# Optimization experiments

Hardware: AMD Instinct MI355X
Metric: run time of the kernel (lower is better)

The kernel has to match this reference:

```python
import jax, jax.numpy as jnp
import numpy as np

NUM_HEADS = 4
KERNEL = 7
DILATION = 1
EMBED = 128
CTX = 256
RANK = 8
HEAD_DIM = EMBED // NUM_HEADS
SCALE = HEAD_DIM ** (-0.5)


def setup_inputs() -> dict:
    key = jax.random.key(0)
    ks = jax.random.split(key, 16)
    B, H, W = 4, 64, 64
    inp = {
        "x": jax.random.normal(ks[0], (B, H, W, EMBED), jnp.float32),
        "context": jax.random.normal(ks[1], (B, CTX), jnp.float32),
        # base QKV linear (torch Linear: y = x @ W.T + b)
        "Wqkv": jax.random.normal(ks[2], (3 * EMBED, EMBED), jnp.float32) * 0.02,
        "bqkv": jax.random.normal(ks[3], (3 * EMBED,), jnp.float32) * 0.02,
        # bilinear LoRA params (init scale 0.01 as in source)
        "A": jax.random.normal(ks[4], (EMBED, RANK), jnp.float32) * 0.01,
        "Blora": jax.random.normal(ks[5], (CTX, RANK), jnp.float32) * 0.01,
        "Vlora": jax.random.normal(ks[6], (3 * EMBED, RANK), jnp.float32) * 0.01,
        # gate MLP: Linear(ctx,16) -> ReLU -> Linear(16,1) -> Sigmoid
        "g1w": jax.random.normal(ks[7], (16, CTX), jnp.float32) * 0.05,
        "g1b": jnp.zeros((16,), jnp.float32),
        "g2w": jnp.full((1, 16), -5.0, jnp.float32) * 0.0 + jax.random.normal(ks[8], (1, 16), jnp.float32) * 0.01 - 5.0 / 16.0,
        "g2b": jnp.full((1,), -5.0, jnp.float32),
        # output projection
        "Wproj": jax.random.normal(ks[9], (EMBED, EMBED), jnp.float32) * 0.02,
        "bproj": jnp.zeros((EMBED,), jnp.float32),
    }
    return inp


def _windows(t, H, W):
    # t: [B, nh, H+2p, W+2p, d] -> [B, nh, H, W, K^2, d]
    ws = []
    for i in range(KERNEL):
        for j in range(KERNEL):
            ws.append(t[:, :, i * DILATION:i * DILATION + H, j * DILATION:j * DILATION + W, :])
    return jnp.stack(ws, axis=4)


def reference(x, context, Wqkv, bqkv, A, Blora, Vlora, g1w, g1b, g2w, g2b, Wproj, bproj):
    B, H, W, C = x.shape
    nh, hd = NUM_HEADS, HEAD_DIM
    # context-modulated QKV: base + alpha * ((xA) * (cB)) V^T
    base = x @ Wqkv.T + bqkv                                   # [B,H,W,3C]
    c_proj = context @ Blora                                   # [B,r]
    delta = ((x @ A) * c_proj[:, None, None, :]) @ Vlora.T     # [B,H,W,3C]
    alpha = jax.nn.sigmoid(jax.nn.relu(context @ g1w.T + g1b) @ g2w.T + g2b)  # [B,1]
    qkv = base + alpha[:, None, None, :] * delta               # [B,H,W,3C]

    qkv = qkv.reshape(B, H, W, 3, nh, hd)
    qkv = jnp.transpose(qkv, (3, 0, 4, 1, 2, 5))               # [3,B,nh,H,W,hd]
    q, k, v = qkv[0], qkv[1], qkv[2]

    pad = DILATION * (KERNEL - 1) // 2
    pw = ((0, 0), (0, 0), (pad, pad), (pad, pad), (0, 0))
    k_p = jnp.pad(k, pw)
    v_p = jnp.pad(v, pw)
    kw = _windows(k_p, H, W)                                   # [B,nh,H,W,K2,hd]
    vw = _windows(v_p, H, W)

    attn = jnp.einsum('bnijd,bnijkd->bnijk', q, kw) * SCALE    # [B,nh,H,W,K2]
    attn = jax.nn.softmax(attn, axis=-1)
    out = jnp.einsum('bnijk,bnijkd->bnijd', attn, vw)          # [B,nh,H,W,hd]

    out = jnp.transpose(out, (0, 2, 3, 1, 4)).reshape(B, H, W, C)
    out = out @ Wproj.T + bproj
    return out
```

## Files before the change

kernel.cpp:

```cpp
#include <hip/hip_runtime.h>
#include <cstddef>

#define CTXDIM 256
#define RANK 8
#define SCALE 0.17677669529663687f
#define WSTRIDE 136

#define XH0 0
#define WF0 26656
#define QS0 35360
#define KL0 44064
#define VT0 61984
#define SMSZ 78368
#define KHEAD 8960
#define VHEAD2 8192

typedef _Float16 half8 __attribute__((ext_vector_type(8)));
typedef _Float16 half2_t __attribute__((ext_vector_type(2)));
typedef float floatx4 __attribute__((ext_vector_type(4)));
typedef float floatx16 __attribute__((ext_vector_type(16)));
typedef int intx4 __attribute__((ext_vector_type(4)));

struct Params {
  const float *x, *ctx, *Wqkv, *bqkv, *A, *Blora, *Vlora;
  const float *g1w, *g1b, *g2w, *g2b, *Wproj, *bproj;
  float* out;
};

__device__ __forceinline__ void compute_cal(const Params& p, int tid,
                                            float* cal_s) {
  const int b = tid >> 6, lane = tid & 63;
  const float c0 = p.ctx[b * CTXDIM + lane];
  const float c1 = p.ctx[b * CTXDIM + 64 + lane];
  const float c2 = p.ctx[b * CTXDIM + 128 + lane];
  const float c3 = p.ctx[b * CTXDIM + 192 + lane];
  float cp[RANK];
#pragma unroll
  for (int r = 0; r < RANK; ++r) {
    float q = c0 * p.Blora[lane * RANK + r] + c1 * p.Blora[(64 + lane) * RANK + r] +
              c2 * p.Blora[(128 + lane) * RANK + r] + c3 * p.Blora[(192 + lane) * RANK + r];
#pragma unroll
    for (int s = 32; s; s >>= 1) q += __shfl_xor(q, s, 64);
    cp[r] = q;
  }
  float gacc = 0.f;
#pragma unroll
  for (int h = 0; h < 16; ++h) {
    float q = c0 * p.g1w[h * CTXDIM + lane] + c1 * p.g1w[h * CTXDIM + 64 + lane] +
              c2 * p.g1w[h * CTXDIM + 128 + lane] + c3 * p.g1w[h * CTXDIM + 192 + lane];
#pragma unroll
    for (int s = 32; s; s >>= 1) q += __shfl_xor(q, s, 64);
    gacc += fmaxf(q + p.g1b[h], 0.f) * p.g2w[h];
  }
  if (lane == 0) {
    const float alpha = 1.f / (1.f + __expf(-(gacc + p.g2b[0])));
#pragma unroll
    for (int r = 0; r < RANK; ++r) cal_s[b * RANK + r] = alpha * cp[r];
  }
}

__device__ __forceinline__ void stage_rows_f16(const float* __restrict__ src,
                                               _Float16* dst, int tid) {
  const int row = tid >> 2;
  const int c0 = (tid & 3) * 32;
  const float* sp = src + (size_t)row * 128 + c0;
  _Float16* dp = dst + row * WSTRIDE + c0;
#pragma unroll
  for (int i = 0; i < 4; ++i) {
    const float4 a = *(const float4*)(sp + i * 8);
    const float4 b = *(const float4*)(sp + i * 8 + 4);
    half8 o;
    o[0] = (_Float16)a.x; o[1] = (_Float16)a.y;
    o[2] = (_Float16)a.z; o[3] = (_Float16)a.w;
    o[4] = (_Float16)b.x; o[5] = (_Float16)b.y;
    o[6] = (_Float16)b.z; o[7] = (_Float16)b.w;
    *(half8*)(dp + i * 8) = o;
  }
}

__device__ __forceinline__ int vta(int d, int k) {
  const int sig = (d + (d >> 3)) & 7;
  return d * 256 + (((k >> 3) ^ sig) << 3) + (k & 7);
}

__device__ __forceinline__ int packh(float x, float y) {
  half2_t h;
  h[0] = (_Float16)x;
  h[1] = (_Float16)y;
  return __builtin_bit_cast(int, h);
}

template <int MT0>
__device__ __forceinline__ floatx16 attn_wave(const _Float16* kls,
                                              const _Float16* vtl,
                                              half8 qb0, half8 qb1,
                                              int m31, int l5, int pi, int pj) {
  const floatx16 zz = {0.f,0.f,0.f,0.f,0.f,0.f,0.f,0.f,
                       0.f,0.f,0.f,0.f,0.f,0.f,0.f,0.f};
  floatx16 acc[5];
#pragma unroll
  for (int mt = 0; mt < 5; ++mt) {
    const int Mt = MT0 + mt;
    const half8 ka0 = *(const half8*)&kls[(Mt * 32 + m31) * 40 + l5 * 8];
    const half8 ka1 = *(const half8*)&kls[(Mt * 32 + m31) * 40 + 16 + l5 * 8];
    floatx16 a = zz;
    a = __builtin_amdgcn_mfma_f32_32x32x16_f16(ka0, qb0, a, 0, 0, 0);
    a = __builtin_amdgcn_mfma_f32_32x32x16_f16(ka1, qb1, a, 0, 0, 0);
    acc[mt] = a;
  }

  bool vR[14];
#pragma unroll
  for (int i = 0; i < 14; ++i) vR[i] = (unsigned)(i - pi) < 7u;
  bool vC[8];
#pragma unroll
  for (int c8 = 0; c8 < 8; ++c8) {
    const int hcv = (c8 & 3) + 8 * (c8 >> 2) + 4 * l5;
    vC[c8] = (unsigned)(hcv - pj) < 7u;
  }

  float mxp[4] = {-1e30f, -1e30f, -1e30f, -1e30f};
#pragma unroll
  for (int mt = 0; mt < 5; ++mt) {
#pragma unroll
    for (int reg = 0; reg < 16; ++reg) {
      const bool v = vR[2 * (MT0 + mt) + (reg >> 3)] &&
                     vC[(reg & 3) + 4 * ((reg >> 2) & 1)];
      const float x = v ? acc[mt][reg] : -1e30f;
      acc[mt][reg] = x;
      mxp[reg & 3] = fmaxf(mxp[reg & 3], x);
    }
  }
  float mx = fmaxf(fmaxf(mxp[0], mxp[1]), fmaxf(mxp[2], mxp[3]));
  mx = fmaxf(mx, __shfl_xor(mx, 32, 64));

  const float SC2 = SCALE * 1.4426950408889634f;
  float sp[4] = {0.f, 0.f, 0.f, 0.f};
#pragma unroll
  for (int mt = 0; mt < 5; ++mt) {
#pragma unroll
    for (int reg = 0; reg < 16; ++reg) {
      const float pv = exp2f((acc[mt][reg] - mx) * SC2);
      acc[mt][reg] = pv;
      sp[reg & 3] += pv;
    }
  }
  float sum = (sp[0] + sp[1]) + (sp[2] + sp[3]);
  sum += __shfl_xor(sum, 32, 64);
  const float inv = 1.f / sum;

  floatx16 oacc = zz;
  const int sigd = (m31 + (m31 >> 3)) & 7;
  const int vbase = m31 * 256;
#pragma unroll
  for (int kk = 0; kk < 10; ++kk) {
    const int ks = MT0 * 2 + kk;
    const int mt = (ks >> 1) - MT0;
    const int r8 = 8 * (ks & 1);
    const int E00 = packh(acc[mt][r8 + 0] * inv, acc[mt][r8 + 1] * inv);
    const int E01 = packh(acc[mt][r8 + 2] * inv, acc[mt][r8 + 3] * inv);
    const int E10 = packh(acc[mt][r8 + 4] * inv, acc[mt][r8 + 5] * inv);
    const int E11 = packh(acc[mt][r8 + 6] * inv, acc[mt][r8 + 7] * inv);
    const int R00 = __shfl_xor(E00, 32, 64);
    const int R01 = __shfl_xor(E01, 32, 64);
    const int R10 = __shfl_xor(E10, 32, 64);
    const int R11 = __shfl_xor(E11, 32, 64);
    const int A0 = l5 ? R10 : E00;
    const int A1 = l5 ? R11 : E01;
    const int A2 = l5 ? E10 : R00;
    const int A3 = l5 ? E11 : R01;
    const intx4 ai = {A0, A1, A2, A3};
    const half8 af = __builtin_bit_cast(half8, ai);
    const half8 vb = *(const half8*)&vtl[vbase + (((2 * ks + l5) ^ sigd) << 3)];
    oacc = __builtin_amdgcn_mfma_f32_32x32x16_f16(af, vb, oacc, 0, 0, 0);
  }
  return oacc;
}

__global__ __launch_bounds__(256, 1) void mono_kernel(Params p) {
  __shared__ __align__(16) _Float16 sm[SMSZ];
  __shared__ float cal_s[32];

  const int bid = blockIdx.x;
  const int tj = bid & 7;
  const int ti = (bid >> 3) & 7;
  const int b  = bid >> 6;
  const int tid = threadIdx.x;
  const int lane = tid & 63;
  const int w = tid >> 6;
  const int m31 = lane & 31;
  const int l5 = lane >> 5;
  const int i0 = ti * 8 - 3;
  const int j0 = tj * 8 - 3;

  _Float16* xh    = sm + XH0;
  _Float16* wfold = sm + WF0;
  _Float16* qs    = sm + QS0;
  _Float16* kls   = sm + KL0;
  _Float16* vtl   = sm + VT0;

  compute_cal(p, tid, cal_s);

  for (int idx = tid; idx < 896; idx += 256) {
    const int d = idx & 31;
    const int kk = idx >> 5;
    const int k = (kk >> 1) * 16 + 14 + (kk & 1);
    const int a = vta(d, k);
    vtl[a] = (_Float16)0.f;
    vtl[VHEAD2 + a] = (_Float16)0.f;
  }

  for (int s = tid; s < 3136; s += 256) {
    const int pp = s >> 4;
    const int d8 = (s & 15) * 8;
    const int hr = pp / 14;
    const int hc = pp - hr * 14;
    const int ii = i0 + hr;
    const int jj = j0 + hc;
    half8 o = {0, 0, 0, 0, 0, 0, 0, 0};
    if ((unsigned)ii < 64u && (unsigned)jj < 64u) {
      const float* sp = p.x + (size_t)(b * 4096 + ii * 64 + jj) * 128 + d8;
      const float4 a = *(const float4*)sp;
      const float4 c = *(const float4*)(sp + 4);
      o[0] = (_Float16)a.x; o[1] = (_Float16)a.y;
      o[2] = (_Float16)a.z; o[3] = (_Float16)a.w;
      o[4] = (_Float16)c.x; o[5] = (_Float16)c.y;
      o[6] = (_Float16)c.z; o[7] = (_Float16)c.w;
    }
    *(half8*)&xh[pp * 136 + d8] = o;
  }

  const int kq = tid & 127;
  const int hgrp = tid >> 7;
  const float4 a0 = *(const float4*)&p.A[kq * RANK];
  const float4 a1 = *(const float4*)&p.A[kq * RANK + 4];
  const float* cb = &cal_s[b * RANK];

  __syncthreads();

  const float t0 = a0.x * cb[0], t1 = a0.y * cb[1];
  const float t2 = a0.z * cb[2], t3 = a0.w * cb[3];
  const float t4 = a1.x * cb[4], t5 = a1.y * cb[5];
  const float t6 = a1.z * cb[6], t7 = a1.w * cb[7];

  const floatx16 zz = {0.f,0.f,0.f,0.f,0.f,0.f,0.f,0.f,
                       0.f,0.f,0.f,0.f,0.f,0.f,0.f,0.f};
  const int sigd = (m31 + (m31 >> 3)) & 7;

  auto FOLD = [&](int n0) {
#pragma unroll
    for (int rr = 0; rr < 32; ++rr) {
      const int row = hgrp * 32 + rr;
      const int o = n0 + row;
      const float4 v0 = *(const float4*)&p.Vlora[o * RANK];
      const float4 v1 = *(const float4*)&p.Vlora[o * RANK + 4];
      float d = t0 * v0.x;
      d = fmaf(t1, v0.y, d);
      d = fmaf(t2, v0.z, d);
      d = fmaf(t3, v0.w, d);
      d = fmaf(t4, v1.x, d);
      d = fmaf(t5, v1.y, d);
      d = fmaf(t6, v1.z, d);
      d = fmaf(t7, v1.w, d);
      wfold[row * WSTRIDE + kq] = (_Float16)(p.Wqkv[o * 128 + kq] + d);
    }
  };

  auto QGEMM = [&](int i) {
    const int n0 = i * 64;
    const int mt = w + 1;
    const float bq0 = p.bqkv[n0 + m31];
    const float bq1 = p.bqkv[n0 + 32 + m31];
    floatx16 c0 = zz, c1 = zz;
    const _Float16* ar  = &xh[(mt * 32 + m31) * 136 + l5 * 8];
    const _Float16* b0r = &wfold[m31 * WSTRIDE + l5 * 8];
    const _Float16* b1r = &wfold[(32 + m31) * WSTRIDE + l5 * 8];
#pragma unroll
    for (int ks = 0; ks < 8; ++ks) {
      const half8 a  = *(const half8*)(ar + ks * 16);
      const half8 f0 = *(const half8*)(b0r + ks * 16);
      const half8 f1 = *(const half8*)(b1r + ks * 16);
      c0 = __builtin_amdgcn_mfma_f32_32x32x16_f16(a, f0, c0, 0, 0, 0);
      c1 = __builtin_amdgcn_mfma_f32_32x32x16_f16(a, f1, c1, 0, 0, 0);
    }
#pragma unroll
    for (int reg = 0; reg < 16; ++reg) {
      const int rowlin = mt * 32 + (reg & 3) + 8 * (reg >> 2) + 4 * l5;
      const int hr = rowlin / 14;
      const int hc = rowlin - hr * 14;
      if ((unsigned)(hr - 3) < 8u && (unsigned)(hc - 3) < 8u) {
        const int px = (hr - 3) * 8 + (hc - 3);
        qs[px * 136 + n0 + m31] = (_Float16)(c0[reg] + bq0);
        qs[px * 136 + n0 + 32 + m31] = (_Float16)(c1[reg] + bq1);
      }
    }
  };

  auto KVGEMM = [&](int i) {
    const int n0 = i * 64;
    const bool isK = (i < 4);
    const float bh0 = p.bqkv[n0 + m31];
    const float bh1 = p.bqkv[n0 + 32 + m31];
#pragma unroll
    for (int mtslot = 0; mtslot < 2; ++mtslot) {
      const int mt = w + 4 * mtslot;
      if (mt < 7) {
        floatx16 c0 = zz, c1 = zz;
        const _Float16* ar  = &xh[(mt * 32 + m31) * 136 + l5 * 8];
        const _Float16* b0r = &wfold[m31 * WSTRIDE + l5 * 8];
        const _Float16* b1r = &wfold[(32 + m31) * WSTRIDE + l5 * 8];
#pragma unroll
        for (int ks = 0; ks < 8; ++ks) {
          const half8 a  = *(const half8*)(ar + ks * 16);
          const half8 f0 = *(const half8*)(b0r + ks * 16);
          const half8 f1 = *(const half8*)(b1r + ks * 16);
          c0 = __builtin_amdgcn_mfma_f32_32x32x16_f16(a, f0, c0, 0, 0, 0);
          c1 = __builtin_amdgcn_mfma_f32_32x32x16_f16(a, f1, c1, 0, 0, 0);
        }
#pragma unroll
        for (int reg = 0; reg < 16; ++reg) {
          const int rowlin = mt * 32 + (reg & 3) + 8 * (reg >> 2) + 4 * l5;
          if (rowlin < 196) {
            const int hr = rowlin / 14;
            const int hc = rowlin - hr * 14;
            const int hp = hr * 16 + hc;
            const bool okimg = (unsigned)(i0 + hr) < 64u &&
                               (unsigned)(j0 + hc) < 64u;
            const float v0 = okimg ? c0[reg] + bh0 : 0.f;
            const float v1 = okimg ? c1[reg] + bh1 : 0.f;
            if (isK) {
              kls[hp * 40 + m31] = (_Float16)v0;
              kls[KHEAD + hp * 40 + m31] = (_Float16)v1;
            } else {
              const int off = (((hp >> 3) ^ sigd) << 3) | (hp & 7);
              vtl[m31 * 256 + off] = (_Float16)v0;
              vtl[VHEAD2 + m31 * 256 + off] = (_Float16)v1;
            }
          }
        }
      }
    }
  };

  FOLD(0);   __syncthreads(); QGEMM(0);  __syncthreads();
  FOLD(64);  __syncthreads(); QGEMM(1);  __syncthreads();
  FOLD(128); __syncthreads(); KVGEMM(2); __syncthreads();
  FOLD(256); __syncthreads(); KVGEMM(4); __syncthreads();

  const int hlq = w >> 1;
  const int half = w & 1;
  const int pixA = half * 32 + m31;
  const int piA = pixA >> 3, pjA = pixA & 7;
  const _Float16* kpp = kls + hlq * KHEAD;
  const _Float16* vpp = vtl + hlq * VHEAD2;

  floatx16 oP1;
  {
    const int hh = hlq;
    const half8 qb0 = *(const half8*)&qs[pixA * 136 + hh * 32 + l5 * 8];
    const half8 qb1 = *(const half8*)&qs[pixA * 136 + hh * 32 + 16 + l5 * 8];
    oP1 = half ? attn_wave<2>(kpp, vpp, qb0, qb1, m31, l5, piA, pjA)
               : attn_wave<0>(kpp, vpp, qb0, qb1, m31, l5, piA, pjA);
  }
  __syncthreads();

  FOLD(192); __syncthreads(); KVGEMM(3); __syncthreads();
  FOLD(320); __syncthreads(); KVGEMM(5); __syncthreads();

  floatx16 oP2;
  {
    const int hh = 2 + hlq;
    const half8 qb0 = *(const half8*)&qs[pixA * 136 + hh * 32 + l5 * 8];
    const half8 qb1 = *(const half8*)&qs[pixA * 136 + hh * 32 + 16 + l5 * 8];
    oP2 = half ? attn_wave<2>(kpp, vpp, qb0, qb1, m31, l5, piA, pjA)
               : attn_wave<0>(kpp, vpp, qb0, qb1, m31, l5, piA, pjA);
  }
  __syncthreads();

  _Float16* at_s = sm + KL0;
  _Float16* wsh  = sm + KL0 + 64 * WSTRIDE;
#pragma unroll
  for (int reg = 0; reg < 16; ++reg) {
    const int rowM = (reg & 3) + 8 * (reg >> 2) + 4 * l5;
    const int pr = half * 32 + rowM;
    at_s[pr * WSTRIDE + hlq * 32 + m31] = (_Float16)oP1[reg];
    at_s[pr * WSTRIDE + (2 + hlq) * 32 + m31] = (_Float16)oP2[reg];
  }
  stage_rows_f16(p.Wproj, wsh, tid);
  stage_rows_f16(p.Wproj + 64 * 128, wsh + 64 * WSTRIDE, tid);
  __syncthreads();

  const int r = lane & 15;
  const int quad = lane >> 4;
  const _Float16* ap = at_s + (w * 16 + r) * WSTRIDE + quad * 8;
  const _Float16* bp = wsh + r * WSTRIDE + quad * 8;
  floatx4 acc[8];
#pragma unroll
  for (int nt = 0; nt < 8; ++nt) acc[nt] = (floatx4){0.f, 0.f, 0.f, 0.f};
#pragma unroll
  for (int kc = 0; kc < 4; ++kc) {
    const half8 a = *(const half8*)(ap + kc * 32);
#pragma unroll
    for (int nt = 0; nt < 8; ++nt) {
      const half8 bf = *(const half8*)(bp + nt * 16 * WSTRIDE + kc * 32);
      acc[nt] = __builtin_amdgcn_mfma_f32_16x16x32_f16(a, bf, acc[nt], 0, 0, 0);
    }
  }

  const int rbase = b * 4096 + (ti * 8 + w * 2 + (quad >> 1)) * 64 +
                    tj * 8 + (quad & 1) * 4;
  float bv[8];
#pragma unroll
  for (int nt = 0; nt < 8; ++nt) bv[nt] = p.bproj[nt * 16 + r];
#pragma unroll
  for (int reg = 0; reg < 4; ++reg) {
    float* cp = p.out + (size_t)(rbase + reg) * 128;
#pragma unroll
    for (int nt = 0; nt < 8; ++nt)
      cp[nt * 16 + r] = acc[nt][reg] + bv[nt];
  }
}

extern "C" void kernel_launch(void* const* d_in, const int* in_sizes, int n_in,
                              void* d_out, int out_size, void* d_ws, size_t ws_size,
                              hipStream_t stream) {
  Params hp;
  hp.x     = (const float*)d_in[0];
  hp.ctx   = (const float*)d_in[1];
  hp.Wqkv  = (const float*)d_in[2];
  hp.bqkv  = (const float*)d_in[3];
  hp.A     = (const float*)d_in[4];
  hp.Blora = (const float*)d_in[5];
  hp.Vlora = (const float*)d_in[6];
  hp.g1w   = (const float*)d_in[7];
  hp.g1b   = (const float*)d_in[8];
  hp.g2w   = (const float*)d_in[9];
  hp.g2b   = (const float*)d_in[10];
  hp.Wproj = (const float*)d_in[11];
  hp.bproj = (const float*)d_in[12];
  hp.out   = (float*)d_out;

  mono_kernel<<<256, 256, 0, stream>>>(hp);
}
```

Before: 51.87 us.

## Double block to 512 threads, keep x rows in registers, run all heads' attention at once

The block grows from 256 to 512 threads (8 waves). The halo x tile is loaded straight into per-wave registers as fp16 MFMA A-fragments rather than staged in shared memory, which frees LDS. That space is used to keep K and V for all four heads at once, with the fourth V head parked in the reused fold buffer, so attention runs once across 8 waves instead of in two 4-wave passes. The fold, Q GEMM and projection work are split across the extra waves. This raises register pressure, since two 8-entry half8 x-row arrays plus saved V values must be held, and adds several cross-phase buffer-reuse dependencies.

New measurement: 46.80 us. 1.11x faster.

```diff
diff --git a/kernel.cpp b/kernel.cpp
--- a/kernel.cpp
+++ b/kernel.cpp
@@ -6,14 +6,13 @@
 #define SCALE 0.17677669529663687f
 #define WSTRIDE 136
 
-#define XH0 0
-#define WF0 26656
-#define QS0 35360
-#define KL0 44064
-#define VT0 61984
-#define SMSZ 78368
+#define WF0 0
+#define QS0 8704
+#define KL0 17408
+#define VT0 53248
+#define SMSZ 77824
 #define KHEAD 8960
-#define VHEAD2 8192
+#define VHEAD 8192
 
 typedef _Float16 half8 __attribute__((ext_vector_type(8)));
 typedef _Float16 half2_t __attribute__((ext_vector_type(2)));
@@ -27,40 +26,8 @@
   float* out;
 };
 
-__device__ __forceinline__ void compute_cal(const Params& p, int tid,
-                                            float* cal_s) {
-  const int b = tid >> 6, lane = tid & 63;
-  const float c0 = p.ctx[b * CTXDIM + lane];
-  const float c1 = p.ctx[b * CTXDIM + 64 + lane];
-  const float c2 = p.ctx[b * CTXDIM + 128 + lane];
-  const float c3 = p.ctx[b * CTXDIM + 192 + lane];
-  float cp[RANK];
-#pragma unroll
-  for (int r = 0; r < RANK; ++r) {
-    float q = c0 * p.Blora[lane * RANK + r] + c1 * p.Blora[(64 + lane) * RANK + r] +
-              c2 * p.Blora[(128 + lane) * RANK + r] + c3 * p.Blora[(192 + lane) * RANK + r];
-#pragma unroll
-    for (int s = 32; s; s >>= 1) q += __shfl_xor(q, s, 64);
-    cp[r] = q;
-  }
-  float gacc = 0.f;
-#pragma unroll
-  for (int h = 0; h < 16; ++h) {
-    float q = c0 * p.g1w[h * CTXDIM + lane] + c1 * p.g1w[h * CTXDIM + 64 + lane] +
-              c2 * p.g1w[h * CTXDIM + 128 + lane] + c3 * p.g1w[h * CTXDIM + 192 + lane];
-#pragma unroll
-    for (int s = 32; s; s >>= 1) q += __shfl_xor(q, s, 64);
-    gacc += fmaxf(q + p.g1b[h], 0.f) * p.g2w[h];
-  }
-  if (lane == 0) {
-    const float alpha = 1.f / (1.f + __expf(-(gacc + p.g2b[0])));
-#pragma unroll
-    for (int r = 0; r < RANK; ++r) cal_s[b * RANK + r] = alpha * cp[r];
-  }
-}
-
-__device__ __forceinline__ void stage_rows_f16(const float* __restrict__ src,
-                                               _Float16* dst, int tid) {
+__device__ __forceinline__ void stage_rows_f16_512(const float* __restrict__ src,
+                                                   _Float16* dst, int tid) {
   const int row = tid >> 2;
   const int c0 = (tid & 3) * 32;
   const float* sp = src + (size_t)row * 128 + c0;
@@ -177,9 +144,9 @@
   return oacc;
 }
 
-__global__ __launch_bounds__(256, 1) void mono_kernel(Params p) {
+__global__ __launch_bounds__(512, 1) void mono_kernel(Params p) {
   __shared__ __align__(16) _Float16 sm[SMSZ];
-  __shared__ float cal_s[32];
+  __shared__ float cal_s[8];
 
   const int bid = blockIdx.x;
   const int tj = bid & 7;
@@ -193,64 +160,101 @@
   const int i0 = ti * 8 - 3;
   const int j0 = tj * 8 - 3;
 
-  _Float16* xh    = sm + XH0;
   _Float16* wfold = sm + WF0;
   _Float16* qs    = sm + QS0;
   _Float16* kls   = sm + KL0;
   _Float16* vtl   = sm + VT0;
 
-  compute_cal(p, tid, cal_s);
-
-  for (int idx = tid; idx < 896; idx += 256) {
-    const int d = idx & 31;
-    const int kk = idx >> 5;
+  const floatx16 zz = {0.f,0.f,0.f,0.f,0.f,0.f,0.f,0.f,
+                       0.f,0.f,0.f,0.f,0.f,0.f,0.f,0.f};
+  const int sigd = (m31 + (m31 >> 3)) & 7;
+
+  auto load_xrow = [&](int rowlin, half8* xr) {
+#pragma unroll
+    for (int ks = 0; ks < 8; ++ks) xr[ks] = (half8){0, 0, 0, 0, 0, 0, 0, 0};
+    if (rowlin < 196) {
+      const int hr = rowlin / 14;
+      const int hc = rowlin - hr * 14;
+      const int ii = i0 + hr;
+      const int jj = j0 + hc;
+      if ((unsigned)ii < 64u && (unsigned)jj < 64u) {
+        const float* xp = p.x + (size_t)(b * 4096 + ii * 64 + jj) * 128 + l5 * 8;
+#pragma unroll
+        for (int ks = 0; ks < 8; ++ks) {
+          const float4 a = *(const float4*)(xp + ks * 16);
+          const float4 c = *(const float4*)(xp + ks * 16 + 4);
+          half8 o;
+          o[0] = (_Float16)a.x; o[1] = (_Float16)a.y;
+          o[2] = (_Float16)a.z; o[3] = (_Float16)a.w;
+          o[4] = (_Float16)c.x; o[5] = (_Float16)c.y;
+          o[6] = (_Float16)c.z; o[7] = (_Float16)c.w;
+          xr[ks] = o;
+        }
+      }
+    }
+  };
+
+  const int mtq = (w & 3) + 1;
+  const int chq = w >> 2;
+  half8 xrq[8];
+  load_xrow(mtq * 32 + m31, xrq);
+
+  if (w == 0) {
+    const float c0 = p.ctx[b * CTXDIM + lane];
+    const float c1 = p.ctx[b * CTXDIM + 64 + lane];
+    const float c2 = p.ctx[b * CTXDIM + 128 + lane];
+    const float c3 = p.ctx[b * CTXDIM + 192 + lane];
+    float cp[RANK];
+#pragma unroll
+    for (int r = 0; r < RANK; ++r) {
+      float q = c0 * p.Blora[lane * RANK + r] + c1 * p.Blora[(64 + lane) * RANK + r] +
+                c2 * p.Blora[(128 + lane) * RANK + r] + c3 * p.Blora[(192 + lane) * RANK + r];
+#pragma unroll
+      for (int s = 32; s; s >>= 1) q += __shfl_xor(q, s, 64);
+      cp[r] = q;
+    }
+    float gacc = 0.f;
+#pragma unroll
+    for (int h = 0; h < 16; ++h) {
+      float q = c0 * p.g1w[h * CTXDIM + lane] + c1 * p.g1w[h * CTXDIM + 64 + lane] +
+                c2 * p.g1w[h * CTXDIM + 128 + lane] + c3 * p.g1w[h * CTXDIM + 192 + lane];
+#pragma unroll
+      for (int s = 32; s; s >>= 1) q += __shfl_xor(q, s, 64);
+      gacc += fmaxf(q + p.g1b[h], 0.f) * p.g2w[h];
+    }
+    if (lane == 0) {
+      const float alpha = 1.f / (1.f + __expf(-(gacc + p.g2b[0])));
+#pragma unroll
+      for (int r = 0; r < RANK; ++r) cal_s[r] = alpha * cp[r];
+    }
+  }
+
+  for (int idx = tid; idx < 2688; idx += 512) {
+    const int hd = idx / 896;
+    const int r2 = idx - hd * 896;
+    const int d = r2 & 31;
+    const int kk = r2 >> 5;
     const int k = (kk >> 1) * 16 + 14 + (kk & 1);
-    const int a = vta(d, k);
-    vtl[a] = (_Float16)0.f;
-    vtl[VHEAD2 + a] = (_Float16)0.f;
-  }
-
-  for (int s = tid; s < 3136; s += 256) {
-    const int pp = s >> 4;
-    const int d8 = (s & 15) * 8;
-    const int hr = pp / 14;
-    const int hc = pp - hr * 14;
-    const int ii = i0 + hr;
-    const int jj = j0 + hc;
-    half8 o = {0, 0, 0, 0, 0, 0, 0, 0};
-    if ((unsigned)ii < 64u && (unsigned)jj < 64u) {
-      const float* sp = p.x + (size_t)(b * 4096 + ii * 64 + jj) * 128 + d8;
-      const float4 a = *(const float4*)sp;
-      const float4 c = *(const float4*)(sp + 4);
-      o[0] = (_Float16)a.x; o[1] = (_Float16)a.y;
-      o[2] = (_Float16)a.z; o[3] = (_Float16)a.w;
-      o[4] = (_Float16)c.x; o[5] = (_Float16)c.y;
-      o[6] = (_Float16)c.z; o[7] = (_Float16)c.w;
-    }
-    *(half8*)&xh[pp * 136 + d8] = o;
+    vtl[hd * VHEAD + vta(d, k)] = (_Float16)0.f;
   }
 
   const int kq = tid & 127;
   const int hgrp = tid >> 7;
   const float4 a0 = *(const float4*)&p.A[kq * RANK];
   const float4 a1 = *(const float4*)&p.A[kq * RANK + 4];
-  const float* cb = &cal_s[b * RANK];
 
   __syncthreads();
 
+  const float* cb = cal_s;
   const float t0 = a0.x * cb[0], t1 = a0.y * cb[1];
   const float t2 = a0.z * cb[2], t3 = a0.w * cb[3];
   const float t4 = a1.x * cb[4], t5 = a1.y * cb[5];
   const float t6 = a1.z * cb[6], t7 = a1.w * cb[7];
 
-  const floatx16 zz = {0.f,0.f,0.f,0.f,0.f,0.f,0.f,0.f,
-                       0.f,0.f,0.f,0.f,0.f,0.f,0.f,0.f};
-  const int sigd = (m31 + (m31 >> 3)) & 7;
-
   auto FOLD = [&](int n0) {
 #pragma unroll
-    for (int rr = 0; rr < 32; ++rr) {
-      const int row = hgrp * 32 + rr;
+    for (int rr = 0; rr < 16; ++rr) {
+      const int row = hgrp * 16 + rr;
       const int o = n0 + row;
       const float4 v0 = *(const float4*)&p.Vlora[o * RANK];
       const float4 v1 = *(const float4*)&p.Vlora[o * RANK + 4];
@@ -268,155 +272,156 @@
 
   auto QGEMM = [&](int i) {
     const int n0 = i * 64;
-    const int mt = w + 1;
-    const float bq0 = p.bqkv[n0 + m31];
-    const float bq1 = p.bqkv[n0 + 32 + m31];
-    floatx16 c0 = zz, c1 = zz;
-    const _Float16* ar  = &xh[(mt * 32 + m31) * 136 + l5 * 8];
-    const _Float16* b0r = &wfold[m31 * WSTRIDE + l5 * 8];
-    const _Float16* b1r = &wfold[(32 + m31) * WSTRIDE + l5 * 8];
+    const int nc = n0 + chq * 32 + m31;
+    const float bq = p.bqkv[nc];
+    floatx16 c = zz;
+    const _Float16* br = &wfold[(chq * 32 + m31) * WSTRIDE + l5 * 8];
 #pragma unroll
     for (int ks = 0; ks < 8; ++ks) {
-      const half8 a  = *(const half8*)(ar + ks * 16);
-      const half8 f0 = *(const half8*)(b0r + ks * 16);
-      const half8 f1 = *(const half8*)(b1r + ks * 16);
-      c0 = __builtin_amdgcn_mfma_f32_32x32x16_f16(a, f0, c0, 0, 0, 0);
-      c1 = __builtin_amdgcn_mfma_f32_32x32x16_f16(a, f1, c1, 0, 0, 0);
+      const half8 f = *(const half8*)(br + ks * 16);
+      c = __builtin_amdgcn_mfma_f32_32x32x16_f16(xrq[ks], f, c, 0, 0, 0);
     }
 #pragma unroll
     for (int reg = 0; reg < 16; ++reg) {
-      const int rowlin = mt * 32 + (reg & 3) + 8 * (reg >> 2) + 4 * l5;
+      const int rowlin = mtq * 32 + (reg & 3) + 8 * (reg >> 2) + 4 * l5;
       const int hr = rowlin / 14;
       const int hc = rowlin - hr * 14;
       if ((unsigned)(hr - 3) < 8u && (unsigned)(hc - 3) < 8u) {
         const int px = (hr - 3) * 8 + (hc - 3);
-        qs[px * 136 + n0 + m31] = (_Float16)(c0[reg] + bq0);
-        qs[px * 136 + n0 + 32 + m31] = (_Float16)(c1[reg] + bq1);
+        qs[px * 136 + nc] = (_Float16)(c[reg] + bq);
       }
     }
   };
 
-  auto KVGEMM = [&](int i) {
-    const int n0 = i * 64;
-    const bool isK = (i < 4);
+  FOLD(0);   __syncthreads(); QGEMM(0); __syncthreads();
+  FOLD(64);  __syncthreads(); QGEMM(1); __syncthreads();
+
+  half8 xrkv[8];
+  load_xrow(w * 32 + m31, xrkv);
+  floatx16 v3save = zz;
+
+  auto KVGEMM = [&](int it) {
+    const int n0 = it * 64;
     const float bh0 = p.bqkv[n0 + m31];
     const float bh1 = p.bqkv[n0 + 32 + m31];
-#pragma unroll
-    for (int mtslot = 0; mtslot < 2; ++mtslot) {
-      const int mt = w + 4 * mtslot;
-      if (mt < 7) {
-        floatx16 c0 = zz, c1 = zz;
-        const _Float16* ar  = &xh[(mt * 32 + m31) * 136 + l5 * 8];
-        const _Float16* b0r = &wfold[m31 * WSTRIDE + l5 * 8];
-        const _Float16* b1r = &wfold[(32 + m31) * WSTRIDE + l5 * 8];
-#pragma unroll
-        for (int ks = 0; ks < 8; ++ks) {
-          const half8 a  = *(const half8*)(ar + ks * 16);
-          const half8 f0 = *(const half8*)(b0r + ks * 16);
-          const half8 f1 = *(const half8*)(b1r + ks * 16);
-          c0 = __builtin_amdgcn_mfma_f32_32x32x16_f16(a, f0, c0, 0, 0, 0);
-          c1 = __builtin_amdgcn_mfma_f32_32x32x16_f16(a, f1, c1, 0, 0, 0);
-        }
-#pragma unroll
-        for (int reg = 0; reg < 16; ++reg) {
-          const int rowlin = mt * 32 + (reg & 3) + 8 * (reg >> 2) + 4 * l5;
-          if (rowlin < 196) {
-            const int hr = rowlin / 14;
-            const int hc = rowlin - hr * 14;
-            const int hp = hr * 16 + hc;
-            const bool okimg = (unsigned)(i0 + hr) < 64u &&
-                               (unsigned)(j0 + hc) < 64u;
-            const float v0 = okimg ? c0[reg] + bh0 : 0.f;
-            const float v1 = okimg ? c1[reg] + bh1 : 0.f;
-            if (isK) {
-              kls[hp * 40 + m31] = (_Float16)v0;
-              kls[KHEAD + hp * 40 + m31] = (_Float16)v1;
-            } else {
-              const int off = (((hp >> 3) ^ sigd) << 3) | (hp & 7);
-              vtl[m31 * 256 + off] = (_Float16)v0;
-              vtl[VHEAD2 + m31 * 256 + off] = (_Float16)v1;
-            }
+    if (w < 7) {
+      floatx16 c0 = zz, c1 = zz;
+      const _Float16* b0r = &wfold[m31 * WSTRIDE + l5 * 8];
+      const _Float16* b1r = &wfold[(32 + m31) * WSTRIDE + l5 * 8];
+#pragma unroll
+      for (int ks = 0; ks < 8; ++ks) {
+        const half8 f0 = *(const half8*)(b0r + ks * 16);
+        const half8 f1 = *(const half8*)(b1r + ks * 16);
+        c0 = __builtin_amdgcn_mfma_f32_32x32x16_f16(xrkv[ks], f0, c0, 0, 0, 0);
+        c1 = __builtin_amdgcn_mfma_f32_32x32x16_f16(xrkv[ks], f1, c1, 0, 0, 0);
+      }
+#pragma unroll
+      for (int reg = 0; reg < 16; ++reg) {
+        const int rowlin = w * 32 + (reg & 3) + 8 * (reg >> 2) + 4 * l5;
+        if (rowlin < 196) {
+          const int hr = rowlin / 14;
+          const int hc = rowlin - hr * 14;
+          const int hp = hr * 16 + hc;
+          const bool ok = (unsigned)(i0 + hr) < 64u && (unsigned)(j0 + hc) < 64u;
+          const float v0 = ok ? c0[reg] + bh0 : 0.f;
+          const float v1 = ok ? c1[reg] + bh1 : 0.f;
+          const int off = (((hp >> 3) ^ sigd) << 3) | (hp & 7);
+          if (it == 2) {
+            kls[hp * 40 + m31] = (_Float16)v0;
+            kls[KHEAD + hp * 40 + m31] = (_Float16)v1;
+          } else if (it == 3) {
+            kls[2 * KHEAD + hp * 40 + m31] = (_Float16)v0;
+            kls[3 * KHEAD + hp * 40 + m31] = (_Float16)v1;
+          } else if (it == 4) {
+            vtl[m31 * 256 + off] = (_Float16)v0;
+            vtl[VHEAD + m31 * 256 + off] = (_Float16)v1;
+          } else {
+            vtl[2 * VHEAD + m31 * 256 + off] = (_Float16)v0;
+            v3save[reg] = v1;
           }
         }
       }
     }
   };
 
-  FOLD(0);   __syncthreads(); QGEMM(0);  __syncthreads();
-  FOLD(64);  __syncthreads(); QGEMM(1);  __syncthreads();
   FOLD(128); __syncthreads(); KVGEMM(2); __syncthreads();
+  FOLD(192); __syncthreads(); KVGEMM(3); __syncthreads();
   FOLD(256); __syncthreads(); KVGEMM(4); __syncthreads();
-
-  const int hlq = w >> 1;
-  const int half = w & 1;
-  const int pixA = half * 32 + m31;
+  FOLD(320); __syncthreads(); KVGEMM(5); __syncthreads();
+
+  for (int idx = tid; idx < 896; idx += 512) {
+    const int d = idx & 31;
+    const int kk = idx >> 5;
+    const int k = (kk >> 1) * 16 + 14 + (kk & 1);
+    wfold[vta(d, k)] = (_Float16)0.f;
+  }
+  if (w < 7) {
+#pragma unroll
+    for (int reg = 0; reg < 16; ++reg) {
+      const int rowlin = w * 32 + (reg & 3) + 8 * (reg >> 2) + 4 * l5;
+      if (rowlin < 196) {
+        const int hr = rowlin / 14;
+        const int hc = rowlin - hr * 14;
+        const int hp = hr * 16 + hc;
+        const int off = (((hp >> 3) ^ sigd) << 3) | (hp & 7);
+        wfold[m31 * 256 + off] = (_Float16)v3save[reg];
+      }
+    }
+  }
+  __syncthreads();
+
+  const int hh = w >> 1;
+  const int half_ = w & 1;
+  const int pixA = half_ * 32 + m31;
   const int piA = pixA >> 3, pjA = pixA & 7;
-  const _Float16* kpp = kls + hlq * KHEAD;
-  const _Float16* vpp = vtl + hlq * VHEAD2;
-
-  floatx16 oP1;
-  {
-    const int hh = hlq;
-    const half8 qb0 = *(const half8*)&qs[pixA * 136 + hh * 32 + l5 * 8];
-    const half8 qb1 = *(const half8*)&qs[pixA * 136 + hh * 32 + 16 + l5 * 8];
-    oP1 = half ? attn_wave<2>(kpp, vpp, qb0, qb1, m31, l5, piA, pjA)
-               : attn_wave<0>(kpp, vpp, qb0, qb1, m31, l5, piA, pjA);
-  }
+  const half8 qb0 = *(const half8*)&qs[pixA * 136 + hh * 32 + l5 * 8];
+  const half8 qb1 = *(const half8*)&qs[pixA * 136 + hh * 32 + 16 + l5 * 8];
+  const _Float16* kpp = kls + hh * KHEAD;
+  const _Float16* vpp = (hh < 3) ? (vtl + hh * VHEAD) : wfold;
+
+  const floatx16 oA = half_ ? attn_wave<2>(kpp, vpp, qb0, qb1, m31, l5, piA, pjA)
+                            : attn_wave<0>(kpp, vpp, qb0, qb1, m31, l5, piA, pjA);
   __syncthreads();
 
-  FOLD(192); __syncthreads(); KVGEMM(3); __syncthreads();
-  FOLD(320); __syncthreads(); KVGEMM(5); __syncthreads();
-
-  floatx16 oP2;
-  {
-    const int hh = 2 + hlq;
-    const half8 qb0 = *(const half8*)&qs[pixA * 136 + hh * 32 + l5 * 8];
-    const half8 qb1 = *(const half8*)&qs[pixA * 136 + hh * 32 + 16 + l5 * 8];
-    oP2 = half ? attn_wave<2>(kpp, vpp, qb0, qb1, m31, l5, piA, pjA)
-               : attn_wave<0>(kpp, vpp, qb0, qb1, m31, l5, piA, pjA);
-  }
-  __syncthreads();
-
-  _Float16* at_s = sm + KL0;
-  _Float16* wsh  = sm + KL0 + 64 * WSTRIDE;
+  _Float16* at_s = kls;
+  _Float16* wsh  = kls + 64 * WSTRIDE;
 #pragma unroll
   for (int reg = 0; reg < 16; ++reg) {
     const int rowM = (reg & 3) + 8 * (reg >> 2) + 4 * l5;
-    const int pr = half * 32 + rowM;
-    at_s[pr * WSTRIDE + hlq * 32 + m31] = (_Float16)oP1[reg];
-    at_s[pr * WSTRIDE + (2 + hlq) * 32 + m31] = (_Float16)oP2[reg];
-  }
-  stage_rows_f16(p.Wproj, wsh, tid);
-  stage_rows_f16(p.Wproj + 64 * 128, wsh + 64 * WSTRIDE, tid);
+    at_s[(half_ * 32 + rowM) * WSTRIDE + hh * 32 + m31] = (_Float16)oA[reg];
+  }
+  stage_rows_f16_512(p.Wproj, wsh, tid);
   __syncthreads();
 
   const int r = lane & 15;
   const int quad = lane >> 4;
-  const _Float16* ap = at_s + (w * 16 + r) * WSTRIDE + quad * 8;
-  const _Float16* bp = wsh + r * WSTRIDE + quad * 8;
-  floatx4 acc[8];
-#pragma unroll
-  for (int nt = 0; nt < 8; ++nt) acc[nt] = (floatx4){0.f, 0.f, 0.f, 0.f};
+  const int rw = w & 3;
+  const int nh = w >> 2;
+  const _Float16* ap = at_s + (rw * 16 + r) * WSTRIDE + quad * 8;
+  const _Float16* bp = wsh + (nh * 64 + r) * WSTRIDE + quad * 8;
+  floatx4 acc[4];
+#pragma unroll
+  for (int nt = 0; nt < 4; ++nt) acc[nt] = (floatx4){0.f, 0.f, 0.f, 0.f};
 #pragma unroll
   for (int kc = 0; kc < 4; ++kc) {
     const half8 a = *(const half8*)(ap + kc * 32);
 #pragma unroll
-    for (int nt = 0; nt < 8; ++nt) {
+    for (int nt = 0; nt < 4; ++nt) {
       const half8 bf = *(const half8*)(bp + nt * 16 * WSTRIDE + kc * 32);
       acc[nt] = __builtin_amdgcn_mfma_f32_16x16x32_f16(a, bf, acc[nt], 0, 0, 0);
     }
   }
 
-  const int rbase = b * 4096 + (ti * 8 + w * 2 + (quad >> 1)) * 64 +
+  const int rbase = b * 4096 + (ti * 8 + rw * 2 + (quad >> 1)) * 64 +
                     tj * 8 + (quad & 1) * 4;
-  float bv[8];
-#pragma unroll
-  for (int nt = 0; nt < 8; ++nt) bv[nt] = p.bproj[nt * 16 + r];
+  float bv[4];
+#pragma unroll
+  for (int nt = 0; nt < 4; ++nt) bv[nt] = p.bproj[nh * 64 + nt * 16 + r];
 #pragma unroll
   for (int reg = 0; reg < 4; ++reg) {
-    float* cp = p.out + (size_t)(rbase + reg) * 128;
-#pragma unroll
-    for (int nt = 0; nt < 8; ++nt)
+    float* cp = p.out + (size_t)(rbase + reg) * 128 + nh * 64;
+#pragma unroll
+    for (int nt = 0; nt < 4; ++nt)
       cp[nt * 16 + r] = acc[nt][reg] + bv[nt];
   }
 }
@@ -440,5 +445,5 @@
   hp.bproj = (const float*)d_in[12];
   hp.out   = (float*)d_out;
 
-  mono_kernel<<<256, 256, 0, stream>>>(hp);
-}
+  mono_kernel<<<256, 512, 0, stream>>>(hp);
+}
```
